# Kernel tuning notes

Measured on AMD Instinct MI355X. Metric: run time of the kernel, lower is better.

## Reference

```python
import jax, jax.numpy as jnp
import numpy as np

B, N, D = 8, 1024, 1024
H = 16
HD = D // H  # 64
SCALE = float(HD) ** -0.5


def setup_inputs() -> dict:
    key = jax.random.key(0)
    k1, k2, k3 = jax.random.split(key, 3)
    x = jax.random.normal(k1, (B, N, D), dtype=jnp.float32)
    W_qkv = jax.random.normal(k2, (D, 3 * D), dtype=jnp.float32) * (D ** -0.5)
    b_qkv = jnp.zeros((3 * D,), dtype=jnp.float32)
    W_o = jax.random.normal(k3, (D, D), dtype=jnp.float32) * (D ** -0.5)
    b_o = jnp.zeros((D,), dtype=jnp.float32)
    return {"x": x, "W_qkv": W_qkv, "b_qkv": b_qkv, "W_o": W_o, "b_o": b_o}


def reference(x, W_qkv, b_qkv, W_o, b_o):
    b, n, _ = x.shape
    qkv = x @ W_qkv + b_qkv                      # (B, N, 3D)
    qkv = qkv.reshape(b, n, H, 3 * HD).transpose(0, 2, 1, 3)  # (B, H, N, 3*HD)
    q, k, v = jnp.split(qkv, 3, axis=-1)          # each (B, H, N, HD)
    attn = jnp.einsum('bhnd,bhmd->bhnm', q, k) * SCALE
    attn = jax.nn.softmax(attn, axis=-1)          # (B, H, N, N); dropout p=0 -> identity
    heads = jnp.einsum('bhnm,bhmd->bhnd', attn, v)
    heads = heads.transpose(0, 2, 1, 3).reshape(b, n, H * HD)  # (B, N, D)
    return heads @ W_o + b_o
```

## Files before the change

### kernel.cpp

```cpp
#include <hip/hip_runtime.h>
#include <hip/hip_bf16.h>

typedef unsigned short ushort_t;
typedef __bf16 bf16x8 __attribute__((ext_vector_type(8)));
typedef float floatx4 __attribute__((ext_vector_type(4)));

#define MFMA(a, b, c) __builtin_amdgcn_mfma_f32_16x16x32_bf16(a, b, c, 0, 0, 0)

__device__ __forceinline__ float b2f(ushort_t u) {
    union { ushort_t u; __hip_bfloat16 h; } cvt; cvt.u = u; return __bfloat162float(cvt.h);
}
__device__ __forceinline__ ushort_t f2b(float f) {
    union { ushort_t u; __hip_bfloat16 h; } cvt; cvt.h = __float2bfloat16(f); return cvt.u;
}

__device__ __forceinline__ void async_copy16(const ushort_t* g, ushort_t* l) {
    __builtin_amdgcn_global_load_lds(
        (const __attribute__((address_space(1))) void*)g,
        (__attribute__((address_space(3))) void*)l, 16, 0, 0);
}

__global__ void convert_x(const float* __restrict__ xin, ushort_t* __restrict__ xb) {
    int i = blockIdx.x * 256 + threadIdx.x;
    const float4* xf = (const float4*)xin;
    float4 a = xf[i * 2], b = xf[i * 2 + 1];
    union { ushort_t s[8]; uint4 v; } p;
    p.s[0] = f2b(a.x); p.s[1] = f2b(a.y); p.s[2] = f2b(a.z); p.s[3] = f2b(a.w);
    p.s[4] = f2b(b.x); p.s[5] = f2b(b.y); p.s[6] = f2b(b.z); p.s[7] = f2b(b.w);
    ((uint4*)xb)[i] = p.v;
}

__global__ void transpose_cvt_qkv(const float* __restrict__ W, ushort_t* __restrict__ Wt) {
    __shared__ float tile[32][33];
    int p0 = blockIdx.x * 32, k0 = blockIdx.y * 32;
    int which = p0 >> 10, rem = p0 & 1023;
    int n0 = (rem >> 6) * 192 + which * 64 + (rem & 63);
    int tx = threadIdx.x, ty = threadIdx.y;
#pragma unroll
    for (int i = 0; i < 4; ++i)
        tile[ty + i * 8][tx] = W[(size_t)(k0 + ty + i * 8) * 3072 + n0 + tx];
    __syncthreads();
#pragma unroll
    for (int i = 0; i < 4; ++i)
        Wt[(size_t)(p0 + ty + i * 8) * 1024 + k0 + tx] = f2b(tile[tx][ty + i * 8]);
}

__global__ void transpose_cvt(const float* __restrict__ W, ushort_t* __restrict__ Wt,
                              int K, int N) {
    __shared__ float tile[32][33];
    int n0 = blockIdx.x * 32, k0 = blockIdx.y * 32;
    int tx = threadIdx.x, ty = threadIdx.y;
#pragma unroll
    for (int i = 0; i < 4; ++i)
        tile[ty + i * 8][tx] = W[(size_t)(k0 + ty + i * 8) * N + n0 + tx];
    __syncthreads();
#pragma unroll
    for (int i = 0; i < 4; ++i)
        Wt[(size_t)(n0 + ty + i * 8) * K + k0 + tx] = f2b(tile[tx][ty + i * 8]);
}

__device__ __forceinline__ int tswz(int n, int m) {
    return n * 128 + (((m >> 3) ^ (n & 15)) << 3) + (m & 7);
}

__global__ __launch_bounds__(256, 3) void gemm_qkv(
    const ushort_t* __restrict__ A,
    const ushort_t* __restrict__ Bt,
    const float* __restrict__ bias,
    ushort_t* __restrict__ Qb, ushort_t* __restrict__ Kb, ushort_t* __restrict__ Vtb) {
    const int K = 1024;
    __shared__ __align__(16) ushort_t SH[16384];
    ushort_t* Alds = SH;
    ushort_t* Blds = SH + 8192;
    int tid = threadIdx.x;
    int wave = tid >> 6, lane = tid & 63;
    int quad = lane >> 4, l16 = lane & 15;
    int wm = (wave >> 1) * 64, wn = (wave & 1) * 64;
    int m0 = blockIdx.x * 128, n0 = blockIdx.y * 128;

    floatx4 acc[4][4] = {};

    int srow[4], scol[4];
#pragma unroll
    for (int p = 0; p < 4; ++p) {
        int slot = (wave * 4 + p) * 64 + lane;
        int row = slot >> 3;
        srow[p] = row;
        scol[p] = ((slot & 7) ^ (row & 7)) * 8;
    }

    for (int kt = 0; kt < 16; ++kt) {
        int k0 = kt * 64;
        __syncthreads();
#pragma unroll
        for (int p = 0; p < 4; ++p) {
            int t = wave * 4 + p;
            async_copy16(&A[(m0 + srow[p]) * K + k0 + scol[p]], &Alds[t * 512]);
            async_copy16(&Bt[(n0 + srow[p]) * K + k0 + scol[p]], &Blds[t * 512]);
        }
        __syncthreads();
#pragma unroll
        for (int ki = 0; ki < 2; ++ki) {
            bf16x8 af[4], bfv[4];
            int sc = ((ki * 4 + quad) ^ (l16 & 7)) * 8;
#pragma unroll
            for (int i = 0; i < 4; ++i) {
                __builtin_memcpy(&af[i],  &Alds[(wm + i * 16 + l16) * 64 + sc], 16);
                __builtin_memcpy(&bfv[i], &Blds[(wn + i * 16 + l16) * 64 + sc], 16);
            }
#pragma unroll
            for (int i = 0; i < 4; ++i)
#pragma unroll
                for (int j = 0; j < 4; ++j)
                    acc[i][j] = MFMA(af[i], bfv[j], acc[i][j]);
        }
    }

    int which = n0 >> 10;
    int b = m0 >> 10;

    if (which < 2) {
        ushort_t* dst = which ? Kb : Qb;
#pragma unroll
        for (int j = 0; j < 4; ++j) {
            int C = n0 + wn + j * 16 + l16;
            int c = C & 1023;
            int h = c >> 6, d = c & 63;
            float bv = bias[((C >> 6) & 15) * 192 + which * 64 + (C & 63)];
            size_t hb = (size_t)(b * 16 + h) * 65536 + d;
#pragma unroll
            for (int i = 0; i < 4; ++i)
#pragma unroll
                for (int g = 0; g < 4; ++g) {
                    int n_tok = (m0 & 1023) + wm + i * 16 + quad * 4 + g;
                    dst[hb + (size_t)n_tok * 64] = f2b(acc[i][j][g] + bv);
                }
        }
    } else {
        __syncthreads();
#pragma unroll
        for (int j = 0; j < 4; ++j) {
            int C = n0 + wn + j * 16 + l16;
            int nl = wn + j * 16 + l16;
            float bv = bias[((C >> 6) & 15) * 192 + 128 + (C & 63)];
#pragma unroll
            for (int i = 0; i < 4; ++i)
#pragma unroll
                for (int g = 0; g < 4; ++g) {
                    int ml = wm + i * 16 + quad * 4 + g;
                    SH[tswz(nl, ml)] = f2b(acc[i][j][g] + bv);
                }
        }
        __syncthreads();
        int r = tid >> 1, half = tid & 1;
        int vcol = (n0 - 2048) + r;
        int h = vcol >> 6, d = vcol & 63;
        size_t base = ((size_t)(b * 16 + h) * 64 + d) * 1024 + (m0 & 1023) + half * 64;
#pragma unroll
        for (int i8 = 0; i8 < 8; ++i8) {
            int chunk = half * 8 + i8;
            uint4 v;
            __builtin_memcpy(&v, &SH[r * 128 + ((chunk ^ (r & 15)) << 3)], 16);
            __builtin_memcpy(&Vtb[base + i8 * 8], &v, 16);
        }
    }
}

__global__ __launch_bounds__(256, 3) void attn(
    const ushort_t* __restrict__ Qb, const ushort_t* __restrict__ Kb,
    const ushort_t* __restrict__ Vtb, ushort_t* __restrict__ heads) {
    __shared__ __align__(16) ushort_t Klds[64 * 64];
    __shared__ __align__(16) ushort_t Vlds[64 * 64];
    __shared__ __align__(16) ushort_t Plds[128 * 76];
    int tid = threadIdx.x;
    int wave = tid >> 6, lane = tid & 63;
    int quad = lane >> 4, l16 = lane & 15;
    int qt = blockIdx.x, h = blockIdx.y, b = blockIdx.z;
    int bh = b * 16 + h;
    const ushort_t* Qh = Qb + (size_t)bh * 65536;
    const ushort_t* Kh = Kb + (size_t)bh * 65536;
    const ushort_t* Vh = Vtb + (size_t)bh * 65536;

    bf16x8 qa[2][2];
#pragma unroll
    for (int mi = 0; mi < 2; ++mi) {
        int qrow = qt * 128 + wave * 32 + mi * 16 + l16;
        __builtin_memcpy(&qa[mi][0], &Qh[qrow * 64 + quad * 8], 16);
        __builtin_memcpy(&qa[mi][1], &Qh[qrow * 64 + 32 + quad * 8], 16);
    }

    floatx4 oacc[2][4] = {};
    floatx4 oext[2] = {};

    bf16x8 onesfrag;
    {
        ushort_t v = (l16 == 0) ? (ushort_t)0x3F80 : (ushort_t)0;
        ushort_t tmp[8] = {v, v, v, v, v, v, v, v};
        __builtin_memcpy(&onesfrag, tmp, 16);
    }

    const float C2 = 0.18033688f;

    int srow[2], scol[2];
#pragma unroll
    for (int p = 0; p < 2; ++p) {
        int slot = (wave * 2 + p) * 64 + lane;
        int row = slot >> 3;
        srow[p] = row;
        scol[p] = ((slot & 7) ^ (row & 7)) * 8;
    }

    for (int kt = 0; kt < 16; ++kt) {
        int key0 = kt * 64;
        __syncthreads();
#pragma unroll
        for (int p = 0; p < 2; ++p) {
            int t = wave * 2 + p;
            async_copy16(&Kh[(key0 + srow[p]) * 64 + scol[p]], &Klds[t * 512]);
            async_copy16(&Vh[srow[p] * 1024 + key0 + scol[p]], &Vlds[t * 512]);
        }
        __syncthreads();

        bf16x8 kf[4][2];
#pragma unroll
        for (int n = 0; n < 4; ++n)
#pragma unroll
            for (int ki = 0; ki < 2; ++ki) {
                int sc = ((ki * 4 + quad) ^ (l16 & 7)) * 8;
                __builtin_memcpy(&kf[n][ki], &Klds[(n * 16 + l16) * 64 + sc], 16);
            }
#pragma unroll
        for (int mi = 0; mi < 2; ++mi) {
#pragma unroll
            for (int n = 0; n < 4; ++n) {
                floatx4 z = {0.f, 0.f, 0.f, 0.f};
#pragma unroll
                for (int ki = 0; ki < 2; ++ki)
                    z = MFMA(kf[n][ki], qa[mi][ki], z);
                union { ushort_t s[4]; double d8; } pk;
#pragma unroll
                for (int g = 0; g < 4; ++g)
                    pk.s[g] = f2b(__builtin_exp2f(fminf(z[g] * C2, 50.f)));
                __builtin_memcpy(
                    &Plds[(wave * 32 + mi * 16 + l16) * 76 + n * 16 + quad * 4], &pk, 8);
            }
        }
        __syncthreads();

        bf16x8 vf[4][2];
#pragma unroll
        for (int n = 0; n < 4; ++n)
#pragma unroll
            for (int ki = 0; ki < 2; ++ki) {
                int sc = ((ki * 4 + quad) ^ (l16 & 7)) * 8;
                __builtin_memcpy(&vf[n][ki], &Vlds[(n * 16 + l16) * 64 + sc], 16);
            }
#pragma unroll
        for (int mi = 0; mi < 2; ++mi) {
            bf16x8 pa[2];
            int prow = wave * 32 + mi * 16 + l16;
#pragma unroll
            for (int ki = 0; ki < 2; ++ki)
                __builtin_memcpy(&pa[ki], &Plds[prow * 76 + ki * 32 + quad * 8], 16);
#pragma unroll
            for (int n = 0; n < 4; ++n)
#pragma unroll
                for (int ki = 0; ki < 2; ++ki)
                    oacc[mi][n] = MFMA(pa[ki], vf[n][ki], oacc[mi][n]);
#pragma unroll
            for (int ki = 0; ki < 2; ++ki)
                oext[mi] = MFMA(pa[ki], onesfrag, oext[mi]);
        }
    }

#pragma unroll
    for (int mi = 0; mi < 2; ++mi)
#pragma unroll
        for (int g = 0; g < 4; ++g) {
            float l = __shfl(oext[mi][g], (lane & 48));
            float inv = 1.f / l;
            int n_tok = qt * 128 + wave * 32 + mi * 16 + quad * 4 + g;
#pragma unroll
            for (int n = 0; n < 4; ++n)
                heads[(size_t)(b * 1024 + n_tok) * 1024 + h * 64 + n * 16 + l16] =
                    f2b(oacc[mi][n][g] * inv);
        }
}

__global__ __launch_bounds__(256, 3) void gemm_out(
    const ushort_t* __restrict__ A,
    const ushort_t* __restrict__ Bt,
    const float* __restrict__ bias,
    float* __restrict__ out) {
    const int K = 1024;
    __shared__ __align__(16) ushort_t Alds[128 * 64];
    __shared__ __align__(16) ushort_t Blds[128 * 64];
    int tid = threadIdx.x;
    int wave = tid >> 6, lane = tid & 63;
    int quad = lane >> 4, l16 = lane & 15;
    int wm = (wave >> 1) * 64, wn = (wave & 1) * 64;
    int m0 = blockIdx.x * 128, n0 = blockIdx.y * 128;

    floatx4 acc[4][4] = {};

    int srow[4], scol[4];
#pragma unroll
    for (int p = 0; p < 4; ++p) {
        int slot = (wave * 4 + p) * 64 + lane;
        int row = slot >> 3;
        srow[p] = row;
        scol[p] = ((slot & 7) ^ (row & 7)) * 8;
    }

    for (int kt = 0; kt < 16; ++kt) {
        int k0 = kt * 64;
        __syncthreads();
#pragma unroll
        for (int p = 0; p < 4; ++p) {
            int t = wave * 4 + p;
            async_copy16(&A[(m0 + srow[p]) * K + k0 + scol[p]], &Alds[t * 512]);
            async_copy16(&Bt[(n0 + srow[p]) * K + k0 + scol[p]], &Blds[t * 512]);
        }
        __syncthreads();
#pragma unroll
        for (int ki = 0; ki < 2; ++ki) {
            bf16x8 af[4], bfv[4];
            int sc = ((ki * 4 + quad) ^ (l16 & 7)) * 8;
#pragma unroll
            for (int i = 0; i < 4; ++i) {
                __builtin_memcpy(&af[i],  &Alds[(wm + i * 16 + l16) * 64 + sc], 16);
                __builtin_memcpy(&bfv[i], &Blds[(wn + i * 16 + l16) * 64 + sc], 16);
            }
#pragma unroll
            for (int i = 0; i < 4; ++i)
#pragma unroll
                for (int j = 0; j < 4; ++j)
                    acc[i][j] = MFMA(af[i], bfv[j], acc[i][j]);
        }
    }

#pragma unroll
    for (int j = 0; j < 4; ++j) {
        int C = n0 + wn + j * 16 + l16;
        float bv = bias[C];
#pragma unroll
        for (int i = 0; i < 4; ++i)
#pragma unroll
            for (int g = 0; g < 4; ++g) {
                int R = m0 + wm + i * 16 + quad * 4 + g;
                out[(size_t)R * 1024 + C] = acc[i][j][g] + bv;
            }
    }
}

extern "C" void kernel_launch(void* const* d_in, const int* in_sizes, int n_in,
                              void* d_out, int out_size, void* d_ws, size_t ws_size,
                              hipStream_t stream) {
    const float* x    = (const float*)d_in[0];
    const float* Wqkv = (const float*)d_in[1];
    const float* bqkv = (const float*)d_in[2];
    const float* Wo   = (const float*)d_in[3];
    const float* bo   = (const float*)d_in[4];

    char* ws = (char*)d_ws;
    const size_t MB = 1u << 20;
    ushort_t* xb    = (ushort_t*)(ws);
    ushort_t* Qb    = (ushort_t*)(ws + 16 * MB);
    ushort_t* Kb    = (ushort_t*)(ws + 32 * MB);
    ushort_t* Vtb   = (ushort_t*)(ws + 48 * MB);
    ushort_t* heads = (ushort_t*)(ws + 64 * MB);
    ushort_t* WqkvT = (ushort_t*)(ws + 64 * MB);
    ushort_t* WoT   = (ushort_t*)(ws);

    convert_x<<<4096, 256, 0, stream>>>(x, xb);
    transpose_cvt_qkv<<<dim3(96, 32), dim3(32, 8), 0, stream>>>(Wqkv, WqkvT);
    gemm_qkv<<<dim3(64, 24), 256, 0, stream>>>(xb, WqkvT, bqkv, Qb, Kb, Vtb);
    attn<<<dim3(8, 16, 8), 256, 0, stream>>>(Qb, Kb, Vtb, heads);
    transpose_cvt<<<dim3(32, 32), dim3(32, 8), 0, stream>>>(Wo, WoT, 1024, 1024);
    gemm_out<<<dim3(64, 8), 256, 0, stream>>>(heads, WoT, bo, (float*)d_out);
}
```

Before: 248.7 us.

## Process two query tiles per attention block with double-buffered K/V prefetch

Each attention block now handles two 128-row query tiles, so every K/V tile loaded into LDS is reused twice and the grid is halved. K/V tiles are double-buffered, with the next tile's async copy issued before the current tile's compute. The barrier between writing and reading P is dropped because each wave only reads its own rows. The softmax scale (including log2e) is folded into Q in the QKV GEMM epilogue, which removes a multiply per score; the cost is higher register and LDS use, with occupancy lowered to 2 blocks per CU and only 512 blocks launched.

```diff
diff --git a/kernel.cpp b/kernel.cpp
--- a/kernel.cpp
+++ b/kernel.cpp
@@ -121,6 +121,7 @@
 
     if (which < 2) {
         ushort_t* dst = which ? Kb : Qb;
+        float sc = which ? 1.0f : 0.18033688f;
 #pragma unroll
         for (int j = 0; j < 4; ++j) {
             int C = n0 + wn + j * 16 + l16;
@@ -133,7 +134,7 @@
 #pragma unroll
                 for (int g = 0; g < 4; ++g) {
                     int n_tok = (m0 & 1023) + wm + i * 16 + quad * 4 + g;
-                    dst[hb + (size_t)n_tok * 64] = f2b(acc[i][j][g] + bv);
+                    dst[hb + (size_t)n_tok * 64] = f2b((acc[i][j][g] + bv) * sc);
                 }
         }
     } else {
@@ -166,31 +167,33 @@
     }
 }
 
-__global__ __launch_bounds__(256, 3) void attn(
+__global__ __launch_bounds__(256, 2) void attn(
     const ushort_t* __restrict__ Qb, const ushort_t* __restrict__ Kb,
     const ushort_t* __restrict__ Vtb, ushort_t* __restrict__ heads) {
-    __shared__ __align__(16) ushort_t Klds[64 * 64];
-    __shared__ __align__(16) ushort_t Vlds[64 * 64];
-    __shared__ __align__(16) ushort_t Plds[128 * 76];
+    __shared__ __align__(16) ushort_t Klds[2][4096];
+    __shared__ __align__(16) ushort_t Vlds[2][4096];
+    __shared__ __align__(16) ushort_t Plds[2][128 * 76];
     int tid = threadIdx.x;
     int wave = tid >> 6, lane = tid & 63;
     int quad = lane >> 4, l16 = lane & 15;
-    int qt = blockIdx.x, h = blockIdx.y, b = blockIdx.z;
+    int h = blockIdx.y, b = blockIdx.z;
     int bh = b * 16 + h;
     const ushort_t* Qh = Qb + (size_t)bh * 65536;
     const ushort_t* Kh = Kb + (size_t)bh * 65536;
     const ushort_t* Vh = Vtb + (size_t)bh * 65536;
 
-    bf16x8 qa[2][2];
-#pragma unroll
-    for (int mi = 0; mi < 2; ++mi) {
-        int qrow = qt * 128 + wave * 32 + mi * 16 + l16;
-        __builtin_memcpy(&qa[mi][0], &Qh[qrow * 64 + quad * 8], 16);
-        __builtin_memcpy(&qa[mi][1], &Qh[qrow * 64 + 32 + quad * 8], 16);
-    }
-
-    floatx4 oacc[2][4] = {};
-    floatx4 oext[2] = {};
+    bf16x8 qa[2][2][2];
+#pragma unroll
+    for (int qt = 0; qt < 2; ++qt)
+#pragma unroll
+        for (int mi = 0; mi < 2; ++mi) {
+            int qrow = (blockIdx.x * 2 + qt) * 128 + wave * 32 + mi * 16 + l16;
+            __builtin_memcpy(&qa[qt][mi][0], &Qh[qrow * 64 + quad * 8], 16);
+            __builtin_memcpy(&qa[qt][mi][1], &Qh[qrow * 64 + 32 + quad * 8], 16);
+        }
+
+    floatx4 oacc[2][2][4] = {};
+    floatx4 oext[2][2] = {};
 
     bf16x8 onesfrag;
     {
@@ -199,8 +202,6 @@
         __builtin_memcpy(&onesfrag, tmp, 16);
     }
 
-    const float C2 = 0.18033688f;
-
     int srow[2], scol[2];
 #pragma unroll
     for (int p = 0; p < 2; ++p) {
@@ -210,16 +211,25 @@
         scol[p] = ((slot & 7) ^ (row & 7)) * 8;
     }
 
+#pragma unroll
+    for (int p = 0; p < 2; ++p) {
+        int t = wave * 2 + p;
+        async_copy16(&Kh[srow[p] * 64 + scol[p]], &Klds[0][t * 512]);
+        async_copy16(&Vh[srow[p] * 1024 + scol[p]], &Vlds[0][t * 512]);
+    }
+
     for (int kt = 0; kt < 16; ++kt) {
-        int key0 = kt * 64;
-        __syncthreads();
-#pragma unroll
-        for (int p = 0; p < 2; ++p) {
-            int t = wave * 2 + p;
-            async_copy16(&Kh[(key0 + srow[p]) * 64 + scol[p]], &Klds[t * 512]);
-            async_copy16(&Vh[srow[p] * 1024 + key0 + scol[p]], &Vlds[t * 512]);
-        }
-        __syncthreads();
+        int cur = kt & 1;
+        __syncthreads();
+        if (kt < 15) {
+            int nk0 = (kt + 1) * 64, nb = cur ^ 1;
+#pragma unroll
+            for (int p = 0; p < 2; ++p) {
+                int t = wave * 2 + p;
+                async_copy16(&Kh[(nk0 + srow[p]) * 64 + scol[p]], &Klds[nb][t * 512]);
+                async_copy16(&Vh[srow[p] * 1024 + nk0 + scol[p]], &Vlds[nb][t * 512]);
+            }
+        }
 
         bf16x8 kf[4][2];
 #pragma unroll
@@ -227,25 +237,26 @@
 #pragma unroll
             for (int ki = 0; ki < 2; ++ki) {
                 int sc = ((ki * 4 + quad) ^ (l16 & 7)) * 8;
-                __builtin_memcpy(&kf[n][ki], &Klds[(n * 16 + l16) * 64 + sc], 16);
-            }
-#pragma unroll
-        for (int mi = 0; mi < 2; ++mi) {
-#pragma unroll
-            for (int n = 0; n < 4; ++n) {
-                floatx4 z = {0.f, 0.f, 0.f, 0.f};
-#pragma unroll
-                for (int ki = 0; ki < 2; ++ki)
-                    z = MFMA(kf[n][ki], qa[mi][ki], z);
-                union { ushort_t s[4]; double d8; } pk;
-#pragma unroll
-                for (int g = 0; g < 4; ++g)
-                    pk.s[g] = f2b(__builtin_exp2f(fminf(z[g] * C2, 50.f)));
-                __builtin_memcpy(
-                    &Plds[(wave * 32 + mi * 16 + l16) * 76 + n * 16 + quad * 4], &pk, 8);
-            }
-        }
-        __syncthreads();
+                __builtin_memcpy(&kf[n][ki], &Klds[cur][(n * 16 + l16) * 64 + sc], 16);
+            }
+#pragma unroll
+        for (int qt = 0; qt < 2; ++qt)
+#pragma unroll
+            for (int mi = 0; mi < 2; ++mi)
+#pragma unroll
+                for (int n = 0; n < 4; ++n) {
+                    floatx4 z = {0.f, 0.f, 0.f, 0.f};
+#pragma unroll
+                    for (int ki = 0; ki < 2; ++ki)
+                        z = MFMA(kf[n][ki], qa[qt][mi][ki], z);
+                    union { ushort_t s[4]; double d8; } pk;
+#pragma unroll
+                    for (int g = 0; g < 4; ++g)
+                        pk.s[g] = f2b(__builtin_exp2f(fminf(z[g], 50.f)));
+                    __builtin_memcpy(
+                        &Plds[qt][(wave * 32 + mi * 16 + l16) * 76 + n * 16 + quad * 4],
+                        &pk, 8);
+                }
 
         bf16x8 vf[4][2];
 #pragma unroll
@@ -253,38 +264,42 @@
 #pragma unroll
             for (int ki = 0; ki < 2; ++ki) {
                 int sc = ((ki * 4 + quad) ^ (l16 & 7)) * 8;
-                __builtin_memcpy(&vf[n][ki], &Vlds[(n * 16 + l16) * 64 + sc], 16);
-            }
-#pragma unroll
-        for (int mi = 0; mi < 2; ++mi) {
-            bf16x8 pa[2];
-            int prow = wave * 32 + mi * 16 + l16;
-#pragma unroll
-            for (int ki = 0; ki < 2; ++ki)
-                __builtin_memcpy(&pa[ki], &Plds[prow * 76 + ki * 32 + quad * 8], 16);
-#pragma unroll
-            for (int n = 0; n < 4; ++n)
+                __builtin_memcpy(&vf[n][ki], &Vlds[cur][(n * 16 + l16) * 64 + sc], 16);
+            }
+#pragma unroll
+        for (int qt = 0; qt < 2; ++qt)
+#pragma unroll
+            for (int mi = 0; mi < 2; ++mi) {
+                bf16x8 pa[2];
+                int prow = wave * 32 + mi * 16 + l16;
 #pragma unroll
                 for (int ki = 0; ki < 2; ++ki)
-                    oacc[mi][n] = MFMA(pa[ki], vf[n][ki], oacc[mi][n]);
-#pragma unroll
-            for (int ki = 0; ki < 2; ++ki)
-                oext[mi] = MFMA(pa[ki], onesfrag, oext[mi]);
-        }
-    }
-
-#pragma unroll
-    for (int mi = 0; mi < 2; ++mi)
-#pragma unroll
-        for (int g = 0; g < 4; ++g) {
-            float l = __shfl(oext[mi][g], (lane & 48));
-            float inv = 1.f / l;
-            int n_tok = qt * 128 + wave * 32 + mi * 16 + quad * 4 + g;
-#pragma unroll
-            for (int n = 0; n < 4; ++n)
-                heads[(size_t)(b * 1024 + n_tok) * 1024 + h * 64 + n * 16 + l16] =
-                    f2b(oacc[mi][n][g] * inv);
-        }
+                    __builtin_memcpy(&pa[ki], &Plds[qt][prow * 76 + ki * 32 + quad * 8], 16);
+#pragma unroll
+                for (int n = 0; n < 4; ++n)
+#pragma unroll
+                    for (int ki = 0; ki < 2; ++ki)
+                        oacc[qt][mi][n] = MFMA(pa[ki], vf[n][ki], oacc[qt][mi][n]);
+#pragma unroll
+                for (int ki = 0; ki < 2; ++ki)
+                    oext[qt][mi] = MFMA(pa[ki], onesfrag, oext[qt][mi]);
+            }
+    }
+
+#pragma unroll
+    for (int qt = 0; qt < 2; ++qt)
+#pragma unroll
+        for (int mi = 0; mi < 2; ++mi)
+#pragma unroll
+            for (int g = 0; g < 4; ++g) {
+                float l = __shfl(oext[qt][mi][g], (lane & 48));
+                float inv = 1.f / l;
+                int n_tok = (blockIdx.x * 2 + qt) * 128 + wave * 32 + mi * 16 + quad * 4 + g;
+#pragma unroll
+                for (int n = 0; n < 4; ++n)
+                    heads[(size_t)(b * 1024 + n_tok) * 1024 + h * 64 + n * 16 + l16] =
+                        f2b(oacc[qt][mi][n][g] * inv);
+            }
 }
 
 __global__ __launch_bounds__(256, 3) void gemm_out(
@@ -375,7 +390,7 @@
     convert_x<<<4096, 256, 0, stream>>>(x, xb);
     transpose_cvt_qkv<<<dim3(96, 32), dim3(32, 8), 0, stream>>>(Wqkv, WqkvT);
     gemm_qkv<<<dim3(64, 24), 256, 0, stream>>>(xb, WqkvT, bqkv, Qb, Kb, Vtb);
-    attn<<<dim3(8, 16, 8), 256, 0, stream>>>(Qb, Kb, Vtb, heads);
+    attn<<<dim3(4, 16, 8), 256, 0, stream>>>(Qb, Kb, Vtb, heads);
     transpose_cvt<<<dim3(32, 32), dim3(32, 8), 0, stream>>>(Wo, WoT, 1024, 1024);
     gemm_out<<<dim3(64, 8), 256, 0, stream>>>(heads, WoT, bo, (float*)d_out);
 }
```

After: 237.1 us. 1.05x faster.
